# Optimization experiments

Measured on AMD Instinct MI355X. Metric: run time of the kernel, lower is better.

Reference implementation:

```python
import jax, jax.numpy as jnp
import numpy as np


def _haar_dwt2(x):
    # x: [b, H, W] -> (ll, lh, hl, hh), each [b, H/2, W/2]; orthonormal 2D Haar
    a = x[:, ::2, ::2]
    b = x[:, ::2, 1::2]
    c = x[:, 1::2, ::2]
    d = x[:, 1::2, 1::2]
    ll = (a + b + c + d) * 0.5
    lh = (a + b - c - d) * 0.5  # detail along rows (frames)
    hl = (a - b + c - d) * 0.5  # detail along cols (features)
    hh = (a - b - c + d) * 0.5
    return ll, lh, hl, hh


def _haar_idwt2(ll, lh, hl, hh):
    a = (ll + lh + hl + hh) * 0.5
    b = (ll + lh - hl - hh) * 0.5
    c = (ll - lh + hl - hh) * 0.5
    d = (ll - lh - hl + hh) * 0.5
    B, H2, W2 = ll.shape
    out = jnp.zeros((B, 2 * H2, 2 * W2), ll.dtype)
    out = out.at[:, ::2, ::2].set(a)
    out = out.at[:, ::2, 1::2].set(b)
    out = out.at[:, 1::2, ::2].set(c)
    out = out.at[:, 1::2, 1::2].set(d)
    return out


def _interp_linear_last(x, m):
    # linear interpolation along last dim from linspace(0,1,n) to linspace(0,1,m)
    n = x.shape[-1]
    pos = jnp.linspace(0.0, 1.0, m, dtype=x.dtype) * (n - 1)
    i0 = jnp.clip(jnp.floor(pos).astype(jnp.int32), 0, n - 2)
    w = pos - i0.astype(x.dtype)
    return x[..., i0] * (1.0 - w) + x[..., i0 + 1] * w


def setup_inputs() -> dict:
    key = jax.random.key(0)
    k0, k1, k2 = jax.random.split(key, 3)
    b, f, c, hidden = 128, 256, 512, 2048
    x = jax.random.normal(k0, (b, f, c), dtype=jnp.float32)
    fc1_w = jax.random.normal(k1, (hidden, c), dtype=jnp.float32) * 0.02
    fc1_b = jnp.zeros((hidden,), dtype=jnp.float32)
    fc2_w = jax.random.normal(k2, (c // 2, hidden), dtype=jnp.float32) * 0.02
    fc2_b = jnp.zeros((c // 2,), dtype=jnp.float32)
    return {"x": x, "fc1_w": fc1_w, "fc1_b": fc1_b, "fc2_w": fc2_w, "fc2_b": fc2_b}


def reference(x, fc1_w, fc1_b, fc2_w, fc2_b):
    b, f, c = x.shape
    ll, lh, hl, hh = _haar_dwt2(x)               # [b, f/2, c/2] each
    ll_up = _interp_linear_last(ll, c)           # [b, f/2, c]
    h = jax.nn.gelu(jnp.einsum('bfc,hc->bfh', ll_up, fc1_w) + fc1_b, approximate=False)
    ll_new = jnp.einsum('bfh,oh->bfo', h, fc2_w) + fc2_b  # [b, f/2, c/2]
    return _haar_idwt2(ll_new, lh, hl, hh)       # [b, f, c]
```

## Files before the change

### kernel.cpp

```cpp
#include <hip/hip_runtime.h>
#include <hip/hip_bf16.h>
#include <stdint.h>

typedef __bf16 bf16;
typedef __attribute__((ext_vector_type(8))) __bf16 bf16x8;
typedef __attribute__((ext_vector_type(4))) float f32x4;

#define B_DIM 128
#define F_DIM 256
#define C_DIM 512
#define HID   2048
#define F2    (F_DIM/2)
#define C2    (C_DIM/2)
#define MROWS (B_DIM*F2)

static constexpr size_t OFF_W1P = 0;
static constexpr size_t OFF_W2  = OFF_W1P + (size_t)HID * C2 * 2;

__device__ __forceinline__ unsigned short bfbits(float f) {
    bf16 h = (bf16)f;
    return __builtin_bit_cast(unsigned short, h);
}

__global__ __launch_bounds__(256) void prep_kernel(
    const float* __restrict__ w1, const float* __restrict__ w2,
    bf16* __restrict__ w1pp, bf16* __restrict__ w2pp)
{
    const int blk = blockIdx.x;
    const int t = threadIdx.x;
    if (blk < 2048) {
        int idx = blk * 256 + t;
        int h = idx >> 8, k = idx & 255;
        const float* wrow = w1 + (size_t)h * C_DIM;
        float acc = 0.f;
        int jlo = (k == 0) ? 0 : (int)((float)(k - 1) * (511.0f / 255.0f));
        int jhi = (int)((float)(k + 1) * (511.0f / 255.0f)) + 1;
        if (jhi > 511) jhi = 511;
        for (int j = jlo; j <= jhi; ++j) {
            float pos = (float)j * (255.0f / 511.0f);
            int i0 = (int)pos;
            if (i0 > 254) i0 = 254;
            float w = pos - (float)i0;
            float coef = (i0 == k) ? (1.0f - w) : ((i0 + 1 == k) ? w : 0.0f);
            acc += coef * wrow[j];
        }
        size_t off = ((((size_t)(h >> 4)) * 8 + (k >> 5)) * 64
                      + ((((k >> 3) & 3) << 4) | (h & 15))) * 8 + (k & 7);
        w1pp[off] = (bf16)acc;
    } else {
        int idx2 = (blk - 2048) * 256 + t;
        int c2 = idx2 >> 11, h = idx2 & 2047;
        float v = w2[(size_t)c2 * HID + h];
        size_t off = ((((size_t)(c2 >> 4)) * 64 + (h >> 5)) * 64
                      + ((((h >> 3) & 3) << 4) | (c2 & 15))) * 8 + (h & 7);
        w2pp[off] = (bf16)v;
    }
}

__global__ __launch_bounds__(512, 4) void fused_mlp(
    const bf16* __restrict__ w1pp, const bf16* __restrict__ w2pp,
    const float* __restrict__ b1, const float* __restrict__ b2,
    const float* __restrict__ x, float* __restrict__ out)
{
    __shared__ __align__(16) char smem[32768];

    const int tid = threadIdx.x;
    const int l   = tid & 63;
    const int wn  = tid >> 6;
    const int lr  = l & 15;
    const int q   = l >> 4;
    const int R0  = blockIdx.x * 32;

    {
        const int rr = tid >> 4;
        const int w0 = tid & 15;
        const int gbf = R0 + rr;
        const float* xr = x + ((size_t)(gbf >> 7) * F_DIM + (size_t)(gbf & 127) * 2) * C_DIM;
        const float* xs = xr + C_DIM;
#pragma unroll
        for (int half = 0; half < 2; ++half) {
            const int w = w0 + half * 16;
            float4 ra[4], rb[4];
#pragma unroll
            for (int i = 0; i < 4; ++i) {
                ra[i] = ((const float4*)xr)[w * 4 + i];
                rb[i] = ((const float4*)xs)[w * 4 + i];
            }
            const float* pa = (const float*)ra;
            const float* pb = (const float*)rb;
            bf16x8 pk;
#pragma unroll
            for (int e = 0; e < 8; ++e)
                pk[e] = (bf16)(0.5f * (pa[2*e] + pa[2*e+1] + pb[2*e] + pb[2*e+1]));
            int slot = (((rr >> 4) * 8 + (w >> 2)) * 64) + ((w & 3) << 4) + (rr & 15);
            *(bf16x8*)(smem + slot * 16) = pk;
        }
    }
    __syncthreads();

    f32x4 acc2[2][2];
#pragma unroll
    for (int m = 0; m < 2; ++m)
#pragma unroll
        for (int n = 0; n < 2; ++n)
            acc2[m][n] = (f32x4){0.f, 0.f, 0.f, 0.f};

    for (int hc = 0; hc < 8; ++hc) {
        f32x4 acc1[2][2];
#pragma unroll
        for (int m = 0; m < 2; ++m)
#pragma unroll
            for (int n = 0; n < 2; ++n)
                acc1[m][n] = (f32x4){0.f, 0.f, 0.f, 0.f};

#pragma unroll
        for (int t = 0; t < 8; ++t) {
            bf16x8 af[2];
#pragma unroll
            for (int m = 0; m < 2; ++m)
                af[m] = *(const bf16x8*)(smem + ((m * 8 + t) * 64 + l) * 16);
#pragma unroll
            for (int n = 0; n < 2; ++n) {
                const int hblk = hc * 16 + wn * 2 + n;
                bf16x8 bw = *(const bf16x8*)(w1pp + (((size_t)hblk * 8 + t) * 64 + l) * 8);
#pragma unroll
                for (int m = 0; m < 2; ++m)
                    acc1[m][n] = __builtin_amdgcn_mfma_f32_16x16x32_bf16(af[m], bw, acc1[m][n], 0, 0, 0);
            }
        }

#pragma unroll
        for (int n = 0; n < 2; ++n) {
            const int col = wn * 32 + n * 16 + lr;
            const float bs = b1[hc * 256 + col];
            const int t2 = col >> 5, qq = (col >> 3) & 3, e = col & 7;
#pragma unroll
            for (int m = 0; m < 2; ++m) {
#pragma unroll
                for (int j = 0; j < 4; ++j) {
                    float v = acc1[m][n][j] + bs;
                    float tt = v * (0.79788456080f + 0.03567740814f * v * v);
                    float ex = __expf(-2.0f * tt);
                    float g = v / (1.0f + ex);
                    const int row = m * 16 + q * 4 + j;
                    int off = ((m * 8 + t2) * 64 + (qq << 4) + (row & 15)) * 8 + e;
                    *(bf16*)(smem + 16384 + off * 2) = (bf16)g;
                }
            }
        }
        __syncthreads();

#pragma unroll
        for (int t = 0; t < 8; ++t) {
            bf16x8 af[2];
#pragma unroll
            for (int m = 0; m < 2; ++m)
                af[m] = *(const bf16x8*)(smem + 16384 + ((m * 8 + t) * 64 + l) * 16);
#pragma unroll
            for (int n = 0; n < 2; ++n) {
                const int c2blk = wn * 2 + n;
                bf16x8 bw = *(const bf16x8*)(w2pp + (((size_t)c2blk * 64 + hc * 8 + t) * 64 + l) * 8);
#pragma unroll
                for (int m = 0; m < 2; ++m)
                    acc2[m][n] = __builtin_amdgcn_mfma_f32_16x16x32_bf16(af[m], bw, acc2[m][n], 0, 0, 0);
            }
        }
        __syncthreads();
    }

#pragma unroll
    for (int n = 0; n < 2; ++n) {
        const int c2 = wn * 32 + n * 16 + lr;
        const float bs = b2[c2];
#pragma unroll
        for (int m = 0; m < 2; ++m) {
#pragma unroll
            for (int j = 0; j < 4; ++j) {
                const int gbf = R0 + m * 16 + q * 4 + j;
                const int b = gbf >> 7, f2 = gbf & 127;
                const float* xr = x + ((size_t)b * F_DIM + (size_t)f2 * 2) * C_DIM;
                float2 p0 = ((const float2*)xr)[c2];
                float2 p1 = ((const float2*)(xr + C_DIM))[c2];
                float a = p0.x, bb = p0.y, cc = p1.x, dd = p1.y;
                float llv = acc2[m][n][j] + bs;
                float lh = 0.5f * (a + bb - cc - dd);
                float hl = 0.5f * (a - bb + cc - dd);
                float hh = 0.5f * (a - bb - cc + dd);
                float2 o0, o1;
                o0.x = 0.5f * (llv + lh + hl + hh);
                o0.y = 0.5f * (llv + lh - hl - hh);
                o1.x = 0.5f * (llv - lh + hl - hh);
                o1.y = 0.5f * (llv - lh - hl + hh);
                float* orow = out + ((size_t)b * F_DIM + (size_t)f2 * 2) * C_DIM;
                ((float2*)orow)[c2] = o0;
                ((float2*)(orow + C_DIM))[c2] = o1;
            }
        }
    }
}

extern "C" void kernel_launch(void* const* d_in, const int* in_sizes, int n_in,
                              void* d_out, int out_size, void* d_ws, size_t ws_size,
                              hipStream_t stream) {
    const float* x     = (const float*)d_in[0];
    const float* fc1_w = (const float*)d_in[1];
    const float* fc1_b = (const float*)d_in[2];
    const float* fc2_w = (const float*)d_in[3];
    const float* fc2_b = (const float*)d_in[4];
    float* out = (float*)d_out;

    char* ws = (char*)d_ws;
    bf16* w1pp = (bf16*)(ws + OFF_W1P);
    bf16* w2pp = (bf16*)(ws + OFF_W2);

    prep_kernel<<<4096, 256, 0, stream>>>(fc1_w, fc2_w, w1pp, w2pp);
    fused_mlp<<<MROWS / 32, 512, 0, stream>>>(w1pp, w2pp, fc1_b, fc2_b, x, out);
}
```

Baseline: 99.94 us.

## Double-buffer weight loads in registers with 64-row tiles and swizzled LDS

Doubles the rows per block to 64, giving 16 waves arranged 4x4, so each weight fragment is reused across more rows and global weight traffic drops. Weight fragments are repacked into a contiguous per-wave order and prefetched one k-step ahead into a double-buffered register set with inline-asm loads and explicit vmcnt waits, so loads overlap the MFMAs. Activations in shared memory use an XOR-swizzled row layout to avoid bank conflicts. GELU outputs are packed in pairs via DPP before being stored, and the inverse-Haar epilogue is simplified algebraically. The costs are more registers per thread and 64KB of LDS per block, which may limit occupancy, plus hand-written wait counts that are fragile.

New measurement: 119.9 us. 20.0% more time.

```diff
diff --git a/kernel.cpp b/kernel.cpp
--- a/kernel.cpp
+++ b/kernel.cpp
@@ -5,22 +5,31 @@
 typedef __bf16 bf16;
 typedef __attribute__((ext_vector_type(8))) __bf16 bf16x8;
 typedef __attribute__((ext_vector_type(4))) float f32x4;
+typedef __attribute__((ext_vector_type(4))) unsigned int u32x4;
 
 #define B_DIM 128
 #define F_DIM 256
 #define C_DIM 512
 #define HID   2048
-#define F2    (F_DIM/2)
-#define C2    (C_DIM/2)
-#define MROWS (B_DIM*F2)
+#define F2    128
+#define C2    256
+#define MROWS 16384
 
 static constexpr size_t OFF_W1P = 0;
-static constexpr size_t OFF_W2  = OFF_W1P + (size_t)HID * C2 * 2;
+static constexpr size_t OFF_W2  = (size_t)HID * C2 * 2;
 
 __device__ __forceinline__ unsigned short bfbits(float f) {
     bf16 h = (bf16)f;
     return __builtin_bit_cast(unsigned short, h);
 }
+
+#define GLOADI(dst, a, imm) \
+    asm volatile("global_load_dwordx4 %0, %1, off offset:%c2" : "=v"(dst) : "v"(a), "n"(imm))
+#define WAITVM4() asm volatile("s_waitcnt vmcnt(4)" ::: "memory")
+#define WAITVM0() asm volatile("s_waitcnt vmcnt(0)" ::: "memory")
+#define SCHED0()  __builtin_amdgcn_sched_barrier(0)
+
+__device__ __forceinline__ bf16x8 asbf(u32x4 v) { return __builtin_bit_cast(bf16x8, v); }
 
 __global__ __launch_bounds__(256) void prep_kernel(
     const float* __restrict__ w1, const float* __restrict__ w2,
@@ -44,32 +53,46 @@
             float coef = (i0 == k) ? (1.0f - w) : ((i0 + 1 == k) ? w : 0.0f);
             acc += coef * wrow[j];
         }
-        size_t off = ((((size_t)(h >> 4)) * 8 + (k >> 5)) * 64
-                      + ((((k >> 3) & 3) << 4) | (h & 15))) * 8 + (k & 7);
-        w1pp[off] = (bf16)acc;
+        size_t fi = ((((size_t)(h >> 8)) * 4 + ((h >> 6) & 3)) * 8 + (k >> 5)) * 4 + ((h >> 4) & 3);
+        w1pp[fi * 512 + (size_t)((((k >> 3) & 3) << 4) | (h & 15)) * 8 + (k & 7)] = (bf16)acc;
     } else {
         int idx2 = (blk - 2048) * 256 + t;
         int c2 = idx2 >> 11, h = idx2 & 2047;
         float v = w2[(size_t)c2 * HID + h];
-        size_t off = ((((size_t)(c2 >> 4)) * 64 + (h >> 5)) * 64
-                      + ((((h >> 3) & 3) << 4) | (c2 & 15))) * 8 + (h & 7);
-        w2pp[off] = (bf16)v;
-    }
-}
-
-__global__ __launch_bounds__(512, 4) void fused_mlp(
+        size_t fi = ((((size_t)(c2 >> 6)) * 8 + (h >> 8)) * 8 + ((h >> 5) & 7)) * 4 + ((c2 >> 4) & 3);
+        w2pp[fi * 512 + (size_t)((((h >> 3) & 3) << 4) | (c2 & 15)) * 8 + (h & 7)] = (bf16)v;
+    }
+}
+
+__global__ __launch_bounds__(1024, 4) void fused_mlp(
     const bf16* __restrict__ w1pp, const bf16* __restrict__ w2pp,
     const float* __restrict__ b1, const float* __restrict__ b2,
     const float* __restrict__ x, float* __restrict__ out)
 {
-    __shared__ __align__(16) char smem[32768];
+    __shared__ __align__(16) char smem[65536];
 
     const int tid = threadIdx.x;
     const int l   = tid & 63;
-    const int wn  = tid >> 6;
+    const int wv  = tid >> 6;
+    const int wm  = wv >> 2;
+    const int wn  = wv & 3;
     const int lr  = l & 15;
     const int q   = l >> 4;
-    const int R0  = blockIdx.x * 32;
+    const int lrx = (lr & 7) << 4;
+    const int R0  = blockIdx.x * 64;
+
+    const char* w1b = (const char*)w1pp;
+    const char* w2b = (const char*)w2pp;
+
+    u32x4 wreg[2][4];
+
+    {
+        const char* a0 = w1b + (size_t)(wn * 8) * 4096 + (size_t)l * 16;
+        GLOADI(wreg[0][0], a0, 0);
+        GLOADI(wreg[0][1], a0, 1024);
+        GLOADI(wreg[0][2], a0, 2048);
+        GLOADI(wreg[0][3], a0, 3072);
+    }
 
     {
         const int rr = tid >> 4;
@@ -92,109 +115,133 @@
 #pragma unroll
             for (int e = 0; e < 8; ++e)
                 pk[e] = (bf16)(0.5f * (pa[2*e] + pa[2*e+1] + pb[2*e] + pb[2*e+1]));
-            int slot = (((rr >> 4) * 8 + (w >> 2)) * 64) + ((w & 3) << 4) + (rr & 15);
-            *(bf16x8*)(smem + slot * 16) = pk;
+            int by = rr * 512 + ((w * 16) ^ ((rr & 7) << 4));
+            *(bf16x8*)(smem + by) = pk;
         }
     }
     __syncthreads();
 
-    f32x4 acc2[2][2];
-#pragma unroll
-    for (int m = 0; m < 2; ++m)
-#pragma unroll
-        for (int n = 0; n < 2; ++n)
-            acc2[m][n] = (f32x4){0.f, 0.f, 0.f, 0.f};
-
+    f32x4 acc2[4];
+#pragma unroll
+    for (int n = 0; n < 4; ++n) acc2[n] = (f32x4){0.f, 0.f, 0.f, 0.f};
+
+    const int arow = (wm * 16 + lr) * 512;
+    const int hrow = 32768 + arow;
+
+#pragma unroll 1
     for (int hc = 0; hc < 8; ++hc) {
-        f32x4 acc1[2][2];
-#pragma unroll
-        for (int m = 0; m < 2; ++m)
-#pragma unroll
-            for (int n = 0; n < 2; ++n)
-                acc1[m][n] = (f32x4){0.f, 0.f, 0.f, 0.f};
-
-#pragma unroll
-        for (int t = 0; t < 8; ++t) {
-            bf16x8 af[2];
-#pragma unroll
-            for (int m = 0; m < 2; ++m)
-                af[m] = *(const bf16x8*)(smem + ((m * 8 + t) * 64 + l) * 16);
-#pragma unroll
-            for (int n = 0; n < 2; ++n) {
-                const int hblk = hc * 16 + wn * 2 + n;
-                bf16x8 bw = *(const bf16x8*)(w1pp + (((size_t)hblk * 8 + t) * 64 + l) * 8);
-#pragma unroll
-                for (int m = 0; m < 2; ++m)
-                    acc1[m][n] = __builtin_amdgcn_mfma_f32_16x16x32_bf16(af[m], bw, acc1[m][n], 0, 0, 0);
-            }
-        }
-
-#pragma unroll
-        for (int n = 0; n < 2; ++n) {
-            const int col = wn * 32 + n * 16 + lr;
-            const float bs = b1[hc * 256 + col];
-            const int t2 = col >> 5, qq = (col >> 3) & 3, e = col & 7;
-#pragma unroll
-            for (int m = 0; m < 2; ++m) {
-#pragma unroll
-                for (int j = 0; j < 4; ++j) {
-                    float v = acc1[m][n][j] + bs;
-                    float tt = v * (0.79788456080f + 0.03567740814f * v * v);
-                    float ex = __expf(-2.0f * tt);
-                    float g = v / (1.0f + ex);
-                    const int row = m * 16 + q * 4 + j;
-                    int off = ((m * 8 + t2) * 64 + (qq << 4) + (row & 15)) * 8 + e;
-                    *(bf16*)(smem + 16384 + off * 2) = (bf16)g;
+        const char* a2 = w2b + (size_t)((wn * 8 + hc) * 8) * 4096 + (size_t)l * 16;
+
+        f32x4 acc1[4];
+#pragma unroll
+        for (int n = 0; n < 4; ++n) acc1[n] = (f32x4){0.f, 0.f, 0.f, 0.f};
+
+        bf16x8 afc = *(const bf16x8*)(smem + arow + ((q * 16) ^ lrx));
+        {
+            const char* a1t = w1b + (size_t)((hc * 4 + wn) * 8) * 4096 + (size_t)l * 16 + 4096;
+#pragma unroll
+            for (int t = 0; t < 8; ++t) {
+                if (t < 7) {
+                    GLOADI(wreg[(t + 1) & 1][0], a1t, 0);
+                    GLOADI(wreg[(t + 1) & 1][1], a1t, 1024);
+                    GLOADI(wreg[(t + 1) & 1][2], a1t, 2048);
+                    GLOADI(wreg[(t + 1) & 1][3], a1t, 3072);
+                    a1t += 4096;
+                } else {
+                    GLOADI(wreg[0][0], a2, 0);
+                    GLOADI(wreg[0][1], a2, 1024);
+                    GLOADI(wreg[0][2], a2, 2048);
+                    GLOADI(wreg[0][3], a2, 3072);
+                }
+                bf16x8 afn;
+                if (t < 7)
+                    afn = *(const bf16x8*)(smem + arow + (((t + 1) * 64 + q * 16) ^ lrx));
+                WAITVM4();
+                SCHED0();
+#pragma unroll
+                for (int n = 0; n < 4; ++n)
+                    acc1[n] = __builtin_amdgcn_mfma_f32_16x16x32_bf16(afc, asbf(wreg[t & 1][n]), acc1[n], 0, 0, 0);
+                if (t < 7) afc = afn;
+            }
+        }
+
+#pragma unroll
+        for (int n = 0; n < 4; ++n) {
+            const float bs = b1[hc * 256 + wn * 64 + n * 16 + lr];
+#pragma unroll
+            for (int j = 0; j < 4; ++j) {
+                float v = acc1[n][j] + bs;
+                float tt = v * (0.79788456080f + 0.03567740814f * v * v);
+                float g = v / (1.0f + __expf(-2.0f * tt));
+                float gp = __builtin_bit_cast(float,
+                    __builtin_amdgcn_mov_dpp(__builtin_bit_cast(int, g), 0xB1, 0xF, 0xF, true));
+                if (!(l & 1)) {
+                    unsigned u = (unsigned)bfbits(g) | ((unsigned)bfbits(gp) << 16);
+                    int row = wm * 16 + q * 4 + j;
+                    int col = wn * 64 + n * 16 + lr;
+                    int by = 32768 + row * 512 + ((col * 2) ^ ((row & 7) << 4));
+                    *(unsigned*)(smem + by) = u;
                 }
             }
         }
         __syncthreads();
 
-#pragma unroll
-        for (int t = 0; t < 8; ++t) {
-            bf16x8 af[2];
-#pragma unroll
-            for (int m = 0; m < 2; ++m)
-                af[m] = *(const bf16x8*)(smem + 16384 + ((m * 8 + t) * 64 + l) * 16);
-#pragma unroll
-            for (int n = 0; n < 2; ++n) {
-                const int c2blk = wn * 2 + n;
-                bf16x8 bw = *(const bf16x8*)(w2pp + (((size_t)c2blk * 64 + hc * 8 + t) * 64 + l) * 8);
-#pragma unroll
-                for (int m = 0; m < 2; ++m)
-                    acc2[m][n] = __builtin_amdgcn_mfma_f32_16x16x32_bf16(af[m], bw, acc2[m][n], 0, 0, 0);
+        bf16x8 hfc = *(const bf16x8*)(smem + hrow + ((q * 16) ^ lrx));
+        {
+            const char* a2t = a2 + 4096;
+#pragma unroll
+            for (int t = 0; t < 8; ++t) {
+                if (t < 7) {
+                    GLOADI(wreg[(t + 1) & 1][0], a2t, 0);
+                    GLOADI(wreg[(t + 1) & 1][1], a2t, 1024);
+                    GLOADI(wreg[(t + 1) & 1][2], a2t, 2048);
+                    GLOADI(wreg[(t + 1) & 1][3], a2t, 3072);
+                    a2t += 4096;
+                }
+                bf16x8 hfn;
+                if (t < 7)
+                    hfn = *(const bf16x8*)(smem + hrow + (((t + 1) * 64 + q * 16) ^ lrx));
+                if (t < 7) {
+                    WAITVM4();
+                } else if (hc < 7) {
+                    const char* a1x = w1b + (size_t)(((hc + 1) * 4 + wn) * 8) * 4096 + (size_t)l * 16;
+                    GLOADI(wreg[0][0], a1x, 0);
+                    GLOADI(wreg[0][1], a1x, 1024);
+                    GLOADI(wreg[0][2], a1x, 2048);
+                    GLOADI(wreg[0][3], a1x, 3072);
+                    WAITVM4();
+                } else {
+                    WAITVM0();
+                }
+                SCHED0();
+#pragma unroll
+                for (int n = 0; n < 4; ++n)
+                    acc2[n] = __builtin_amdgcn_mfma_f32_16x16x32_bf16(hfc, asbf(wreg[t & 1][n]), acc2[n], 0, 0, 0);
+                if (t < 7) hfc = hfn;
             }
         }
         __syncthreads();
     }
 
 #pragma unroll
-    for (int n = 0; n < 2; ++n) {
-        const int c2 = wn * 32 + n * 16 + lr;
+    for (int n = 0; n < 4; ++n) {
+        const int c2 = wn * 64 + n * 16 + lr;
         const float bs = b2[c2];
 #pragma unroll
-        for (int m = 0; m < 2; ++m) {
-#pragma unroll
-            for (int j = 0; j < 4; ++j) {
-                const int gbf = R0 + m * 16 + q * 4 + j;
-                const int b = gbf >> 7, f2 = gbf & 127;
-                const float* xr = x + ((size_t)b * F_DIM + (size_t)f2 * 2) * C_DIM;
-                float2 p0 = ((const float2*)xr)[c2];
-                float2 p1 = ((const float2*)(xr + C_DIM))[c2];
-                float a = p0.x, bb = p0.y, cc = p1.x, dd = p1.y;
-                float llv = acc2[m][n][j] + bs;
-                float lh = 0.5f * (a + bb - cc - dd);
-                float hl = 0.5f * (a - bb + cc - dd);
-                float hh = 0.5f * (a - bb - cc + dd);
-                float2 o0, o1;
-                o0.x = 0.5f * (llv + lh + hl + hh);
-                o0.y = 0.5f * (llv + lh - hl - hh);
-                o1.x = 0.5f * (llv - lh + hl - hh);
-                o1.y = 0.5f * (llv - lh - hl + hh);
-                float* orow = out + ((size_t)b * F_DIM + (size_t)f2 * 2) * C_DIM;
-                ((float2*)orow)[c2] = o0;
-                ((float2*)(orow + C_DIM))[c2] = o1;
-            }
+        for (int j = 0; j < 4; ++j) {
+            const int gbf = R0 + wm * 16 + q * 4 + j;
+            const int b = gbf >> 7, f2 = gbf & 127;
+            const float* xr = x + ((size_t)b * F_DIM + (size_t)f2 * 2) * C_DIM;
+            float2 p0 = ((const float2*)xr)[c2];
+            float2 p1 = ((const float2*)(xr + C_DIM))[c2];
+            float llo = 0.5f * (p0.x + p0.y + p1.x + p1.y);
+            float d = 0.5f * ((acc2[n][j] + bs) - llo);
+            float2 o0, o1;
+            o0.x = p0.x + d; o0.y = p0.y + d;
+            o1.x = p1.x + d; o1.y = p1.y + d;
+            float* orow = out + ((size_t)b * F_DIM + (size_t)f2 * 2) * C_DIM;
+            ((float2*)orow)[c2] = o0;
+            ((float2*)(orow + C_DIM))[c2] = o1;
         }
     }
 }
@@ -214,5 +261,5 @@
     bf16* w2pp = (bf16*)(ws + OFF_W2);
 
     prep_kernel<<<4096, 256, 0, stream>>>(fc1_w, fc2_w, w1pp, w2pp);
-    fused_mlp<<<MROWS / 32, 512, 0, stream>>>(w1pp, w2pp, fc1_b, fc2_b, x, out);
-}
+    fused_mlp<<<MROWS / 64, 1024, 0, stream>>>(w1pp, w2pp, fc1_b, fc2_b, x, out);
+}
```

## Use 32x32 MFMA with 64-row tiles and register-prefetched weights

Applied to the files above, without the earlier changes.

Moves the fused MLP from 16x16x32 to 32x32x16 bf16 MFMA and doubles the rows per block to 64, so each weight fragment loaded from global memory is reused across more rows. Hidden chunks grow to 512. The GELU output is packed in pairs via DPP and written to LDS in two halves, interleaved with the second GEMM. Weight fragments are prefetched four deep in registers, and the inverse Haar epilogue is simplified algebraically. The costs are larger LDS (64KB), lower occupancy (launch bounds 2), and more barriers per chunk.

Result: slower. 108.8 us (+8.8%).

```diff
diff --git a/kernel.cpp b/kernel.cpp
--- a/kernel.cpp
+++ b/kernel.cpp
@@ -3,19 +3,18 @@
 #include <stdint.h>
 
 typedef __bf16 bf16;
-typedef __attribute__((ext_vector_type(8))) __bf16 bf16x8;
-typedef __attribute__((ext_vector_type(4))) float f32x4;
+typedef __attribute__((ext_vector_type(8)))  __bf16 bf16x8;
+typedef __attribute__((ext_vector_type(16))) float  f32x16;
 
 #define B_DIM 128
 #define F_DIM 256
 #define C_DIM 512
 #define HID   2048
-#define F2    (F_DIM/2)
-#define C2    (C_DIM/2)
-#define MROWS (B_DIM*F2)
-
-static constexpr size_t OFF_W1P = 0;
-static constexpr size_t OFF_W2  = OFF_W1P + (size_t)HID * C2 * 2;
+#define C2    256
+#define MROWS 16384
+
+static constexpr size_t OFF_W1 = 0;
+static constexpr size_t OFF_W2 = 1u << 20;
 
 __device__ __forceinline__ unsigned short bfbits(float f) {
     bf16 h = (bf16)f;
@@ -44,153 +43,158 @@
             float coef = (i0 == k) ? (1.0f - w) : ((i0 + 1 == k) ? w : 0.0f);
             acc += coef * wrow[j];
         }
-        size_t off = ((((size_t)(h >> 4)) * 8 + (k >> 5)) * 64
-                      + ((((k >> 3) & 3) << 4) | (h & 15))) * 8 + (k & 7);
-        w1pp[off] = (bf16)acc;
+        size_t frag = (size_t)(h >> 5) * 16 + (k >> 4);
+        size_t lane = (size_t)(((k >> 3) & 1) << 5 | (h & 31));
+        w1pp[frag * 512 + lane * 8 + (k & 7)] = (bf16)acc;
     } else {
         int idx2 = (blk - 2048) * 256 + t;
-        int c2 = idx2 >> 11, h = idx2 & 2047;
-        float v = w2[(size_t)c2 * HID + h];
-        size_t off = ((((size_t)(c2 >> 4)) * 64 + (h >> 5)) * 64
-                      + ((((h >> 3) & 3) << 4) | (c2 & 15))) * 8 + (h & 7);
-        w2pp[off] = (bf16)v;
-    }
-}
-
-__global__ __launch_bounds__(512, 4) void fused_mlp(
+        int c2 = idx2 >> 11, hid = idx2 & 2047;
+        float v = w2[(size_t)c2 * HID + hid];
+        size_t frag = (size_t)(c2 >> 5) * 128 + (hid >> 4);
+        size_t lane = (size_t)(((hid >> 3) & 1) << 5 | (c2 & 31));
+        w2pp[frag * 512 + lane * 8 + (hid & 7)] = (bf16)v;
+    }
+}
+
+__global__ __launch_bounds__(512, 2) void fused_mlp(
     const bf16* __restrict__ w1pp, const bf16* __restrict__ w2pp,
     const float* __restrict__ b1, const float* __restrict__ b2,
     const float* __restrict__ x, float* __restrict__ out)
 {
-    __shared__ __align__(16) char smem[32768];
+    __shared__ __align__(16) char smem[65536];
+    char* hsm = smem + 32768;
 
     const int tid = threadIdx.x;
     const int l   = tid & 63;
-    const int wn  = tid >> 6;
-    const int lr  = l & 15;
-    const int q   = l >> 4;
-    const int R0  = blockIdx.x * 32;
+    const int wv  = tid >> 6;
+    const int R0  = blockIdx.x * 64;
+    const char* w1B = (const char*)w1pp;
+    const char* w2B = (const char*)w2pp;
 
     {
-        const int rr = tid >> 4;
-        const int w0 = tid & 15;
-        const int gbf = R0 + rr;
-        const float* xr = x + ((size_t)(gbf >> 7) * F_DIM + (size_t)(gbf & 127) * 2) * C_DIM;
-        const float* xs = xr + C_DIM;
-#pragma unroll
-        for (int half = 0; half < 2; ++half) {
-            const int w = w0 + half * 16;
-            float4 ra[4], rb[4];
+        const int r  = tid >> 3;
+        const int rg = r >> 5;
+        const int gbf = R0 + r;
+        const float* xr0 = x + ((size_t)(gbf >> 7) * F_DIM + (size_t)(gbf & 127) * 2) * C_DIM;
+        const float* xr1 = xr0 + C_DIM;
+#pragma unroll
+        for (int jj = 0; jj < 4; ++jj) {
+            int j = (tid & 7) * 4 + jj;
+            float4 a[4], b[4];
 #pragma unroll
             for (int i = 0; i < 4; ++i) {
-                ra[i] = ((const float4*)xr)[w * 4 + i];
-                rb[i] = ((const float4*)xs)[w * 4 + i];
-            }
-            const float* pa = (const float*)ra;
-            const float* pb = (const float*)rb;
+                a[i] = ((const float4*)xr0)[j * 4 + i];
+                b[i] = ((const float4*)xr1)[j * 4 + i];
+            }
+            const float* pa = (const float*)a;
+            const float* pb = (const float*)b;
             bf16x8 pk;
 #pragma unroll
             for (int e = 0; e < 8; ++e)
                 pk[e] = (bf16)(0.5f * (pa[2*e] + pa[2*e+1] + pb[2*e] + pb[2*e+1]));
-            int slot = (((rr >> 4) * 8 + (w >> 2)) * 64) + ((w & 3) << 4) + (rr & 15);
-            *(bf16x8*)(smem + slot * 16) = pk;
+            int kf   = j >> 1;
+            int lane = ((j & 1) << 5) | (r & 31);
+            *(bf16x8*)(smem + (((kf * 2 + rg) * 64) + lane) * 16) = pk;
         }
     }
     __syncthreads();
 
-    f32x4 acc2[2][2];
-#pragma unroll
-    for (int m = 0; m < 2; ++m)
-#pragma unroll
-        for (int n = 0; n < 2; ++n)
-            acc2[m][n] = (f32x4){0.f, 0.f, 0.f, 0.f};
-
-    for (int hc = 0; hc < 8; ++hc) {
-        f32x4 acc1[2][2];
-#pragma unroll
-        for (int m = 0; m < 2; ++m)
-#pragma unroll
-            for (int n = 0; n < 2; ++n)
-                acc1[m][n] = (f32x4){0.f, 0.f, 0.f, 0.f};
-
-#pragma unroll
-        for (int t = 0; t < 8; ++t) {
-            bf16x8 af[2];
-#pragma unroll
-            for (int m = 0; m < 2; ++m)
-                af[m] = *(const bf16x8*)(smem + ((m * 8 + t) * 64 + l) * 16);
-#pragma unroll
-            for (int n = 0; n < 2; ++n) {
-                const int hblk = hc * 16 + wn * 2 + n;
-                bf16x8 bw = *(const bf16x8*)(w1pp + (((size_t)hblk * 8 + t) * 64 + l) * 8);
-#pragma unroll
-                for (int m = 0; m < 2; ++m)
-                    acc1[m][n] = __builtin_amdgcn_mfma_f32_16x16x32_bf16(af[m], bw, acc1[m][n], 0, 0, 0);
-            }
-        }
-
-#pragma unroll
-        for (int n = 0; n < 2; ++n) {
-            const int col = wn * 32 + n * 16 + lr;
-            const float bs = b1[hc * 256 + col];
-            const int t2 = col >> 5, qq = (col >> 3) & 3, e = col & 7;
-#pragma unroll
-            for (int m = 0; m < 2; ++m) {
-#pragma unroll
-                for (int j = 0; j < 4; ++j) {
-                    float v = acc1[m][n][j] + bs;
-                    float tt = v * (0.79788456080f + 0.03567740814f * v * v);
-                    float ex = __expf(-2.0f * tt);
-                    float g = v / (1.0f + ex);
-                    const int row = m * 16 + q * 4 + j;
-                    int off = ((m * 8 + t2) * 64 + (qq << 4) + (row & 15)) * 8 + e;
-                    *(bf16*)(smem + 16384 + off * 2) = (bf16)g;
-                }
-            }
-        }
-        __syncthreads();
-
-#pragma unroll
-        for (int t = 0; t < 8; ++t) {
-            bf16x8 af[2];
-#pragma unroll
-            for (int m = 0; m < 2; ++m)
-                af[m] = *(const bf16x8*)(smem + 16384 + ((m * 8 + t) * 64 + l) * 16);
-#pragma unroll
-            for (int n = 0; n < 2; ++n) {
-                const int c2blk = wn * 2 + n;
-                bf16x8 bw = *(const bf16x8*)(w2pp + (((size_t)c2blk * 64 + hc * 8 + t) * 64 + l) * 8);
-#pragma unroll
-                for (int m = 0; m < 2; ++m)
-                    acc2[m][n] = __builtin_amdgcn_mfma_f32_16x16x32_bf16(af[m], bw, acc2[m][n], 0, 0, 0);
-            }
-        }
-        __syncthreads();
-    }
-
-#pragma unroll
-    for (int n = 0; n < 2; ++n) {
-        const int c2 = wn * 32 + n * 16 + lr;
+    f32x16 acc2_0{}, acc2_1{};
+
+    auto geluwrite = [&](const f32x16& A, int nf, int rg, int hc) {
+        const float bs = b1[hc * 512 + wv * 64 + nf * 32 + (l & 31)];
+#pragma unroll
+        for (int reg = 0; reg < 16; ++reg) {
+            float v = A[reg] + bs;
+            float tt = v * (0.79788456080f + 0.03567740814f * v * v);
+            float g = v / (1.0f + __expf(-2.0f * tt));
+            float gp = __builtin_bit_cast(float,
+                __builtin_amdgcn_mov_dpp(__builtin_bit_cast(int, g), 0xB1, 0xF, 0xF, true));
+            if (!(l & 1)) {
+                unsigned u = (unsigned)bfbits(g) | ((unsigned)bfbits(gp) << 16);
+                int crow  = (reg & 3) + 8 * (reg >> 2) + 4 * (l >> 5);
+                int kf2   = (wv & 3) * 4 + nf * 2 + ((l & 31) >> 4);
+                int lane2 = ((l >> 3) & 1) << 5 | crow;
+                *(unsigned*)(hsm + ((kf2 * 2 + rg) * 64 + lane2) * 16 + (l & 7) * 2) = u;
+            }
+        }
+    };
+
+    auto g2half = [&](int hc, int hs) {
+        bf16x8 wr2[4];
+        const char* w2f = w2B + ((size_t)(wv * 128 + hc * 32 + hs * 16)) * 1024 + (size_t)l * 16;
+#pragma unroll
+        for (int i = 0; i < 4; ++i) wr2[i] = *(const bf16x8*)(w2f + i * 1024);
+#pragma unroll
+        for (int ks = 0; ks < 16; ++ks) {
+            bf16x8 h0 = *(const bf16x8*)(hsm + ((ks * 2 + 0) * 64 + l) * 16);
+            bf16x8 h1 = *(const bf16x8*)(hsm + ((ks * 2 + 1) * 64 + l) * 16);
+            acc2_0 = __builtin_amdgcn_mfma_f32_32x32x16_bf16(h0, wr2[ks & 3], acc2_0, 0, 0, 0);
+            acc2_1 = __builtin_amdgcn_mfma_f32_32x32x16_bf16(h1, wr2[ks & 3], acc2_1, 0, 0, 0);
+            if (ks + 4 < 16)
+                wr2[ks & 3] = *(const bf16x8*)(w2f + (ks + 4) * 1024);
+        }
+    };
+
+#pragma unroll 1
+    for (int hc = 0; hc < 4; ++hc) {
+        f32x16 a1_00{}, a1_01{}, a1_10{}, a1_11{};
+        bf16x8 wr0[4], wr1[4];
+        const char* w1f0 = w1B + ((size_t)((hc * 16 + wv * 2 + 0) * 16)) * 1024 + (size_t)l * 16;
+        const char* w1f1 = w1B + ((size_t)((hc * 16 + wv * 2 + 1) * 16)) * 1024 + (size_t)l * 16;
+#pragma unroll
+        for (int i = 0; i < 4; ++i) {
+            wr0[i] = *(const bf16x8*)(w1f0 + i * 1024);
+            wr1[i] = *(const bf16x8*)(w1f1 + i * 1024);
+        }
+#pragma unroll
+        for (int ks = 0; ks < 16; ++ks) {
+            bf16x8 a0 = *(const bf16x8*)(smem + ((ks * 2 + 0) * 64 + l) * 16);
+            bf16x8 a1 = *(const bf16x8*)(smem + ((ks * 2 + 1) * 64 + l) * 16);
+            a1_00 = __builtin_amdgcn_mfma_f32_32x32x16_bf16(a0, wr0[ks & 3], a1_00, 0, 0, 0);
+            a1_01 = __builtin_amdgcn_mfma_f32_32x32x16_bf16(a1, wr0[ks & 3], a1_01, 0, 0, 0);
+            a1_10 = __builtin_amdgcn_mfma_f32_32x32x16_bf16(a0, wr1[ks & 3], a1_10, 0, 0, 0);
+            a1_11 = __builtin_amdgcn_mfma_f32_32x32x16_bf16(a1, wr1[ks & 3], a1_11, 0, 0, 0);
+            if (ks + 4 < 16) {
+                wr0[ks & 3] = *(const bf16x8*)(w1f0 + (ks + 4) * 1024);
+                wr1[ks & 3] = *(const bf16x8*)(w1f1 + (ks + 4) * 1024);
+            }
+        }
+
+        if (wv < 4) {
+            geluwrite(a1_00, 0, 0, hc); geluwrite(a1_01, 0, 1, hc);
+            geluwrite(a1_10, 1, 0, hc); geluwrite(a1_11, 1, 1, hc);
+        }
+        __syncthreads();
+        g2half(hc, 0);
+        __syncthreads();
+        if (wv >= 4) {
+            geluwrite(a1_00, 0, 0, hc); geluwrite(a1_01, 0, 1, hc);
+            geluwrite(a1_10, 1, 0, hc); geluwrite(a1_11, 1, 1, hc);
+        }
+        __syncthreads();
+        g2half(hc, 1);
+        __syncthreads();
+    }
+
+    {
+        const int c2 = wv * 32 + (l & 31);
         const float bs = b2[c2];
 #pragma unroll
-        for (int m = 0; m < 2; ++m) {
-#pragma unroll
-            for (int j = 0; j < 4; ++j) {
-                const int gbf = R0 + m * 16 + q * 4 + j;
-                const int b = gbf >> 7, f2 = gbf & 127;
+        for (int rg = 0; rg < 2; ++rg) {
+            const f32x16& A = rg ? acc2_1 : acc2_0;
+#pragma unroll
+            for (int reg = 0; reg < 16; ++reg) {
+                int R = R0 + rg * 32 + (reg & 3) + 8 * (reg >> 2) + 4 * (l >> 5);
+                int b = R >> 7, f2 = R & 127;
                 const float* xr = x + ((size_t)b * F_DIM + (size_t)f2 * 2) * C_DIM;
                 float2 p0 = ((const float2*)xr)[c2];
                 float2 p1 = ((const float2*)(xr + C_DIM))[c2];
-                float a = p0.x, bb = p0.y, cc = p1.x, dd = p1.y;
-                float llv = acc2[m][n][j] + bs;
-                float lh = 0.5f * (a + bb - cc - dd);
-                float hl = 0.5f * (a - bb + cc - dd);
-                float hh = 0.5f * (a - bb - cc + dd);
+                float llo = 0.5f * (p0.x + p0.y + p1.x + p1.y);
+                float d = 0.5f * ((A[reg] + bs) - llo);
                 float2 o0, o1;
-                o0.x = 0.5f * (llv + lh + hl + hh);
-                o0.y = 0.5f * (llv + lh - hl - hh);
-                o1.x = 0.5f * (llv - lh + hl - hh);
-                o1.y = 0.5f * (llv - lh - hl + hh);
+                o0.x = p0.x + d; o0.y = p0.y + d;
+                o1.x = p1.x + d; o1.y = p1.y + d;
                 float* orow = out + ((size_t)b * F_DIM + (size_t)f2 * 2) * C_DIM;
                 ((float2*)orow)[c2] = o0;
                 ((float2*)(orow + C_DIM))[c2] = o1;
@@ -210,9 +214,9 @@
     float* out = (float*)d_out;
 
     char* ws = (char*)d_ws;
-    bf16* w1pp = (bf16*)(ws + OFF_W1P);
+    bf16* w1pp = (bf16*)(ws + OFF_W1);
     bf16* w2pp = (bf16*)(ws + OFF_W2);
 
     prep_kernel<<<4096, 256, 0, stream>>>(fc1_w, fc2_w, w1pp, w2pp);
-    fused_mlp<<<MROWS / 32, 512, 0, stream>>>(w1pp, w2pp, fc1_b, fc2_b, x, out);
-}
+    fused_mlp<<<MROWS / 64, 512, 0, stream>>>(w1pp, w2pp, fc1_b, fc2_b, x, out);
+}
```
